# Kernel optimization log

Measured on AMD Instinct MI355X. Metric: run time of the kernel, lower is better.

Reference implementation:

```python
import jax, jax.numpy as jnp
import numpy as np

MAX_DEG = 10
MIN_DEG = 0
N_FEAT = 128
NB_FILTER = 128
BATCH = 128
DEG_COUNT = 30000                      # atoms per degree bucket (static)
N_ATOMS = (MAX_DEG + 1) * DEG_COUNT    # 330000, atoms sorted by degree (deg0 first)
NB_AFFINE = 3 * MAX_DEG + (2 - MIN_DEG)  # 32
EPS = 1e-5


def setup_inputs() -> dict:
    key = jax.random.key(0)
    ks = jax.random.split(key, 16)
    atoms = jax.random.normal(ks[0], (N_ATOMS, N_FEAT), dtype=jnp.float32)
    membership = jax.random.randint(ks[1], (N_ATOMS,), 0, BATCH)
    # deg_slice[d] = [start, count] for degree d (atoms sorted by degree)
    deg_slice = jnp.stack([jnp.arange(MAX_DEG + 1) * DEG_COUNT,
                           jnp.full((MAX_DEG + 1,), DEG_COUNT)], axis=1)
    inp = {"atoms": atoms, "deg_slice": deg_slice, "membership": membership}
    for d in range(1, MAX_DEG + 1):
        inp[f"adj{d}"] = jax.random.randint(ks[1 + d], (DEG_COUNT, d), 0, N_ATOMS)
    glorot = (2.0 / (N_FEAT + NB_FILTER)) ** 0.5
    inp["W"] = jax.random.normal(ks[12], (NB_AFFINE, N_FEAT, NB_FILTER), dtype=jnp.float32) * glorot
    inp["b"] = jnp.zeros((NB_AFFINE, NB_FILTER), dtype=jnp.float32)
    inp["gamma"] = jnp.ones((NB_FILTER,), dtype=jnp.float32)
    inp["beta"] = jnp.zeros((NB_FILTER,), dtype=jnp.float32)
    return inp


def _self_slice(atoms, deg):
    return jax.lax.dynamic_slice_in_dim(atoms, deg * DEG_COUNT, DEG_COUNT, axis=0)


def _norm(x, gamma, beta):
    m = jnp.mean(x, axis=-1, keepdims=True)
    std = jnp.sqrt(jnp.var(x, axis=-1, keepdims=True) + EPS)
    return gamma * ((x - m) / (std + EPS)) + beta


def _forward(atoms, W, b, gamma, beta, membership, adjs):
    # W consumption order matches the TF iterator: for deg=1..max_deg -> (rel, self),
    # then deg0 self at index 2*MAX_DEG, then gather affines deg1..max_deg, deg0 last.
    rel_outs = [None] * (MAX_DEG + 1)
    gather_outs = [None] * (MAX_DEG + 1)
    for d in range(1, MAX_DEG + 1):
        neigh = jnp.sum(atoms[adjs[d - 1]], axis=1)          # (COUNT, F) gather+sum
        self_a = _self_slice(atoms, d)                        # (COUNT, F)
        i_rel, i_self = 2 * (d - 1), 2 * d - 1
        rel_outs[d] = (neigh @ W[i_rel] + b[i_rel]) + (self_a @ W[i_self] + b[i_self])
        i_g = 2 * MAX_DEG + d
        gather_outs[d] = self_a @ W[i_g] + b[i_g]
    self0 = _self_slice(atoms, 0)
    rel_outs[0] = self0 @ W[2 * MAX_DEG] + b[2 * MAX_DEG]
    gather_outs[0] = self0 @ W[NB_AFFINE - 1] + b[NB_AFFINE - 1]

    activated = jnp.concatenate(rel_outs, axis=0)             # (N_ATOMS, NB_FILTER)
    gathered = jnp.concatenate(gather_outs, axis=0)           # (N_ATOMS, NB_FILTER)
    # graph_gather: per-molecule sum (dynamic_partition + reduce_sum)
    atom_gather = jax.ops.segment_sum(gathered, membership, num_segments=BATCH)

    xn = _norm(activated, gamma, beta)                        # per-row "BN" as in source
    yn = _norm(atom_gather, gamma, beta)
    # gather_node: per-molecule max of normalized atom features
    g = jax.ops.segment_max(xn, membership, num_segments=BATCH)
    return xn, yn, g


def reference(atoms, deg_slice, membership, adj1, adj2, adj3, adj4, adj5,
              adj6, adj7, adj8, adj9, adj10, W, b, gamma, beta):
    adjs = (adj1, adj2, adj3, adj4, adj5, adj6, adj7, adj8, adj9, adj10)
    return _forward(atoms, W, b, gamma, beta, membership, adjs)
```

## Files before the change

kernel.cpp:

```cpp
#include <hip/hip_runtime.h>
#include <stdint.h>

#define MAX_DEG   10
#define DEG_COUNT 30000
#define N_ATOMS   330000
#define NF        128
#define BATCH     128
#define SORT_BLOCKS 256
#define SORT_CHUNK  1290
#define NB_BUILD  1408
#define NB_CAST   41250
#define NSLICES   4

typedef __attribute__((ext_vector_type(8))) short bf16x8;
typedef __attribute__((ext_vector_type(4))) float f32x4;
typedef __attribute__((ext_vector_type(2))) float f32x2;

__device__ __forceinline__ float bf2f(unsigned short h) {
  union { unsigned u; float f; } v; v.u = ((unsigned)h) << 16; return v.f;
}
__device__ __forceinline__ unsigned short f2bf(float f) {
  union { float f; unsigned u; } v; v.f = f;
  unsigned u = v.u;
  unsigned r = (u + 0x7fffu + ((u >> 16) & 1u)) >> 16;
  return (unsigned short)r;
}

struct AdjPtrs { const int* p[10]; };

#define NEG_INF_BITS 0xFF800000

__global__ __launch_bounds__(256) void k_prep(
    const float* __restrict__ W,
    const float* __restrict__ b,
    const f32x4* __restrict__ atoms4,
    const int* __restrict__ membership,
    unsigned short* __restrict__ BcatT,
    float* __restrict__ biascat,
    ushort4* __restrict__ dst4,
    int* __restrict__ blockHistT)
{
  const int bx = blockIdx.x;
  const int tid = threadIdx.x;
  __shared__ int bins[BATCH];

  if (bx < NB_BUILD) {
    int idx = bx * 256 + tid;
    if (idx < 11 * 128) {
      int d = idx >> 7, n = idx & 127;
      float f = (d >= 1) ? (b[(2 * (d - 1)) * 128 + n] + b[(2 * d - 1) * 128 + n])
                         : b[20 * 128 + n];
      biascat[idx] = f;
    }
    if (idx < 11 * 128 * 256) {
      int d = idx >> 15;
      int rem = idx & 32767;
      int n = rem >> 8;
      int k = rem & 255;
      float v;
      if (k < 128) {
        v = (d >= 1) ? W[(2 * (d - 1)) * 16384 + k * 128 + n] : 0.f;
      } else {
        int ks = k - 128;
        int wi = (d >= 1) ? (2 * d - 1) : 20;
        v = W[wi * 16384 + ks * 128 + n];
      }
      BcatT[idx] = f2bf(v);
    }
  } else if (bx < NB_BUILD + NB_CAST) {
    size_t i = (size_t)(bx - NB_BUILD) * 256 + tid;
    f32x4 v = __builtin_nontemporal_load(atoms4 + i);
    ushort4 o;
    o.x = f2bf(v[0]); o.y = f2bf(v[1]); o.z = f2bf(v[2]); o.w = f2bf(v[3]);
    dst4[i] = o;
  } else {
    int bh = bx - NB_BUILD - NB_CAST;
    if (tid < BATCH) bins[tid] = 0;
    __syncthreads();
    int lo = bh * SORT_CHUNK, hi = min(lo + SORT_CHUNK, N_ATOMS);
    for (int i = lo + tid; i < hi; i += 256)
      atomicAdd(&bins[membership[i]], 1);
    __syncthreads();
    if (tid < BATCH) blockHistT[tid * 256 + bh] = bins[tid];
  }
}

__global__ __launch_bounds__(256) void k_scan(
    const int* __restrict__ blockHistT,
    int* __restrict__ relOffT,
    int* __restrict__ tot)
{
  const int m = blockIdx.x;
  const int tid = threadIdx.x;
  __shared__ int ws[4];
  int v = blockHistT[m * 256 + tid];
  int x = v;
#pragma unroll
  for (int o = 1; o < 64; o <<= 1) {
    int t = __shfl_up(x, o, 64);
    if ((tid & 63) >= o) x += t;
  }
  if ((tid & 63) == 63) ws[tid >> 6] = x;
  __syncthreads();
  int wb = 0;
  for (int w = 0; w < (tid >> 6); ++w) wb += ws[w];
  int incl = wb + x;
  relOffT[m * 256 + tid] = incl - v;
  if (tid == 255) tot[m] = incl;
}

__global__ __launch_bounds__(256) void k_scatter(
    const int* __restrict__ membership,
    const int* __restrict__ relOffT,
    const int* __restrict__ tot,
    int* __restrict__ perm)
{
  __shared__ int totS[BATCH], baseS[BATCH], bins[BATCH];
  const int tid = threadIdx.x;
  if (tid < BATCH) totS[tid] = tot[tid];
  __syncthreads();
  if (tid == 0) {
    int a = 0;
    for (int i = 0; i < BATCH; ++i) { baseS[i] = a; a += totS[i]; }
  }
  __syncthreads();
  if (tid < BATCH) bins[tid] = baseS[tid] + relOffT[tid * 256 + blockIdx.x];
  __syncthreads();
  int lo = blockIdx.x * SORT_CHUNK, hi = min(lo + SORT_CHUNK, N_ATOMS);
  for (int i = lo + tid; i < hi; i += 256) {
    int m = membership[i];
    int pos = atomicAdd(&bins[m], 1);
    perm[pos] = i;
  }
}

template<int D>
__device__ __forceinline__ void nsum_row1(const unsigned* __restrict__ atomsU,
                                          const int* __restrict__ abase,
                                          unsigned* __restrict__ NS,
                                          int iloc, int rclamp, int lane) {
  const int* a = abase + (size_t)rclamp * D;
  int myIdx = (lane < D) ? a[lane] : 0;
  unsigned xs[D];
#pragma unroll
  for (int j = 0; j < D; ++j) {
    int nbr = __shfl(myIdx, j, 64);
    xs[j] = atomsU[(size_t)nbr * 64 + lane];
  }
  float s0 = 0.f, s1 = 0.f;
#pragma unroll
  for (int j = 0; j < D; ++j) {
    s0 += bf2f((unsigned short)(xs[j] & 0xffff));
    s1 += bf2f((unsigned short)(xs[j] >> 16));
  }
  int sw = lane ^ ((iloc & 7) << 2);
  NS[(size_t)iloc * 64 + sw] = (unsigned)f2bf(s0) | ((unsigned)f2bf(s1) << 16);
}

template<int D>
__device__ __forceinline__ void nsum_phase0(const unsigned* __restrict__ atomsU,
                                            const int* __restrict__ abase,
                                            unsigned* __restrict__ NS,
                                            int rowTile, int wave, int lane) {
  for (int it = 0; it < 4; ++it) {
    int iloc = wave * 16 + it * 4;
    int r0 = rowTile * 128 + iloc;
    if (r0 + 3 < DEG_COUNT) {
      const int* a = abase + (size_t)r0 * D;
      int myIdx = (lane < 4 * D) ? a[lane] : 0;
      unsigned xs[4 * D];
#pragma unroll
      for (int j = 0; j < 4 * D; ++j) {
        int nbr = __shfl(myIdx, j, 64);
        xs[j] = atomsU[(size_t)nbr * 64 + lane];
      }
#pragma unroll
      for (int rr = 0; rr < 4; ++rr) {
        float s0 = 0.f, s1 = 0.f;
#pragma unroll
        for (int j = rr * D; j < (rr + 1) * D; ++j) {
          s0 += bf2f((unsigned short)(xs[j] & 0xffff));
          s1 += bf2f((unsigned short)(xs[j] >> 16));
        }
        int il = iloc + rr;
        int sw = lane ^ ((il & 7) << 2);
        NS[(size_t)il * 64 + sw] = (unsigned)f2bf(s0) | ((unsigned)f2bf(s1) << 16);
      }
    } else {
#pragma unroll
      for (int rr = 0; rr < 4; ++rr) {
        int r = r0 + rr;
        int rc = (r > DEG_COUNT - 1) ? (DEG_COUNT - 1) : r;
        nsum_row1<D>(atomsU, abase, NS, iloc + rr, rc, lane);
      }
    }
  }
}

__global__ __launch_bounds__(512, 4) void k_gemm(
    const unsigned short* __restrict__ atomsBf,
    AdjPtrs adj,
    const unsigned short* __restrict__ BcatT,
    const float* __restrict__ biascat,
    const float* __restrict__ gamma,
    const float* __restrict__ beta,
    float* __restrict__ out0)
{
  const int d = blockIdx.y;
  const int rowTile = blockIdx.x;
  const int tid = threadIdx.x;
  const int lane = tid & 63;
  const int wave = tid >> 6;
  const int m16 = lane & 15;
  const int g = lane >> 4;

  __shared__ unsigned short Bs[128 * 256];
  unsigned* NS = (unsigned*)Bs;

  const unsigned short* Bd = BcatT + d * 32768;
  const unsigned* atomsU = (const unsigned*)atomsBf;

  const int rowBase = rowTile * 128 + wave * 16;
  bf16x8 af[8];
  {
    int rbL = rowBase + m16; if (rbL > DEG_COUNT - 1) rbL = DEG_COUNT - 1;
    size_t gr = (size_t)d * DEG_COUNT + rbL;
#pragma unroll
    for (int ks = 4; ks < 8; ++ks)
      af[ks] = *(const bf16x8*)(atomsBf + gr * 128 + (ks - 4) * 32 + g * 8);
  }

  if (d > 0) {
    const int* abase = adj.p[d - 1];
    switch (d) {
      case 1:  nsum_phase0<1>(atomsU, abase, NS, rowTile, wave, lane); break;
      case 2:  nsum_phase0<2>(atomsU, abase, NS, rowTile, wave, lane); break;
      case 3:  nsum_phase0<3>(atomsU, abase, NS, rowTile, wave, lane); break;
      case 4:  nsum_phase0<4>(atomsU, abase, NS, rowTile, wave, lane); break;
      case 5:  nsum_phase0<5>(atomsU, abase, NS, rowTile, wave, lane); break;
      case 6:  nsum_phase0<6>(atomsU, abase, NS, rowTile, wave, lane); break;
      case 7:  nsum_phase0<7>(atomsU, abase, NS, rowTile, wave, lane); break;
      case 8:  nsum_phase0<8>(atomsU, abase, NS, rowTile, wave, lane); break;
      case 9:  nsum_phase0<9>(atomsU, abase, NS, rowTile, wave, lane); break;
      default: nsum_phase0<10>(atomsU, abase, NS, rowTile, wave, lane); break;
    }
    __syncthreads();
    const char* nsb = (const char*)NS;
    const int rowb = (wave * 16 + m16) * 256;
    const int sw = (m16 & 7) << 4;
#pragma unroll
    for (int ks = 0; ks < 4; ++ks)
      af[ks] = *(const bf16x8*)(nsb + ((rowb + ks * 64 + g * 16) ^ sw));
    __syncthreads();
  } else {
    bf16x8 z = {0, 0, 0, 0, 0, 0, 0, 0};
#pragma unroll
    for (int ks = 0; ks < 4; ++ks) af[ks] = z;
  }

#pragma unroll
  for (int it = 0; it < 8; ++it) {
    int flat = it * 512 + tid;
    int row = flat >> 5;
    int c = flat & 31;
    uint4 v = *(const uint4*)(Bd + row * 256 + c * 8);
    int kb = (c * 16) ^ ((row & 7) << 4);
    *(uint4*)((char*)Bs + row * 512 + kb) = v;
  }

  __syncthreads();

  const int ldsMask = (m16 & 7) << 4;

  f32x4 acc[8];
#pragma unroll
  for (int ct = 0; ct < 8; ++ct) acc[ct] = (f32x4){0.f, 0.f, 0.f, 0.f};

#pragma unroll
  for (int ct = 0; ct < 8; ++ct) {
    const char* bbase = (const char*)Bs + (ct * 16 + m16) * 512;
    bf16x8 bf[8];
#pragma unroll
    for (int ks = 0; ks < 8; ++ks)
      bf[ks] = *(const bf16x8*)(bbase + ((ks * 64 + g * 16) ^ ldsMask));
#pragma unroll
    for (int ks = 0; ks < 8; ++ks)
      acc[ct] = __builtin_amdgcn_mfma_f32_16x16x32_bf16(af[ks], bf[ks], acc[ct], 0, 0, 0);
  }

  float bias_[8], gam[8], bet[8];
#pragma unroll
  for (int ct = 0; ct < 8; ++ct) {
    bias_[ct] = biascat[d * 128 + ct * 16 + m16];
    gam[ct] = gamma[ct * 16 + m16];
    bet[ct] = beta[ct * 16 + m16];
  }

#pragma unroll
  for (int ct = 0; ct < 8; ++ct)
#pragma unroll
    for (int r = 0; r < 4; ++r) acc[ct][r] += bias_[ct];

  float s[4], qq[4];
#pragma unroll
  for (int r = 0; r < 4; ++r) {
    s[r] = 0.f; qq[r] = 0.f;
#pragma unroll
    for (int ct = 0; ct < 8; ++ct) {
      float v = acc[ct][r];
      s[r] += v; qq[r] += v * v;
    }
  }
#pragma unroll
  for (int off = 8; off >= 1; off >>= 1) {
#pragma unroll
    for (int r = 0; r < 4; ++r) {
      s[r]  += __shfl_xor(s[r],  off, 64);
      qq[r] += __shfl_xor(qq[r], off, 64);
    }
  }

#pragma unroll
  for (int r = 0; r < 4; ++r) {
    int rb = rowBase + g * 4 + r;
    float mean = s[r] * (1.0f / 128.0f);
    float var  = qq[r] * (1.0f / 128.0f) - mean * mean;
    float inv  = 1.0f / (sqrtf(var + 1e-5f) + 1e-5f);
    if (rb < DEG_COUNT) {
      size_t grow = (size_t)d * DEG_COUNT + rb;
#pragma unroll
      for (int ct = 0; ct < 8; ++ct)
        out0[grow * 128 + ct * 16 + m16] = gam[ct] * ((acc[ct][r] - mean) * inv) + bet[ct];
    }
  }
}

__global__ __launch_bounds__(512) void k_mreduce(
    const f32x2* __restrict__ xnV,
    const unsigned* __restrict__ atomsU,
    const int* __restrict__ perm,
    const int* __restrict__ tot,
    float* __restrict__ Spart,
    int* __restrict__ cntPart,
    float2* __restrict__ pmax4)
{
  const int m = blockIdx.x >> 2;
  const int s = blockIdx.x & 3;
  const int wave = threadIdx.x >> 6, lane = threadIdx.x & 63;

  __shared__ float S[8][11][128];
  __shared__ int C[8][11];
  __shared__ float2 maxT[8][64];
  __shared__ int totS[BATCH];
  __shared__ int rangeS[2];
  for (int e = lane; e < 11 * 128; e += 64) S[wave][e >> 7][e & 127] = 0.f;
  if (lane < 11) C[wave][lane] = 0;
  if (threadIdx.x < BATCH) totS[threadIdx.x] = tot[threadIdx.x];
  __syncthreads();
  if (threadIdx.x == 0) {
    int a = 0;
    for (int i = 0; i < m; ++i) a += totS[i];
    rangeS[0] = a; rangeS[1] = totS[m];
  }
  __syncthreads();
  const int b0 = rangeS[0], cnt = rangeS[1];
  const int lo = b0 + (cnt * s) / NSLICES;
  const int hi = b0 + (cnt * (s + 1)) / NSLICES;

  const float NEG_INF = __int_as_float((int)NEG_INF_BITS);
  float mx0 = NEG_INF, mx1 = NEG_INF;

  for (int i = lo + wave * 2; i < hi; i += 16) {
    int r0 = perm[i];
    bool has1 = (i + 1 < hi);
    int r1 = has1 ? perm[i + 1] : r0;
    f32x2 x0 = __builtin_nontemporal_load(xnV + (size_t)r0 * 64 + lane);
    unsigned a0 = __builtin_nontemporal_load(atomsU + (size_t)r0 * 64 + lane);
    f32x2 x1 = __builtin_nontemporal_load(xnV + (size_t)r1 * 64 + lane);
    unsigned a1 = __builtin_nontemporal_load(atomsU + (size_t)r1 * 64 + lane);
    int d0 = r0 / DEG_COUNT;
    mx0 = fmaxf(mx0, x0[0]);
    mx1 = fmaxf(mx1, x0[1]);
    S[wave][d0][lane]      += bf2f((unsigned short)(a0 & 0xffff));
    S[wave][d0][64 + lane] += bf2f((unsigned short)(a0 >> 16));
    if (lane == 0) C[wave][d0]++;
    if (has1) {
      int d1 = r1 / DEG_COUNT;
      mx0 = fmaxf(mx0, x1[0]);
      mx1 = fmaxf(mx1, x1[1]);
      S[wave][d1][lane]      += bf2f((unsigned short)(a1 & 0xffff));
      S[wave][d1][64 + lane] += bf2f((unsigned short)(a1 >> 16));
      if (lane == 0) C[wave][d1]++;
    }
  }
  maxT[wave][lane] = make_float2(mx0, mx1);
  __syncthreads();

  if (threadIdx.x < 64) {
    int l = threadIdx.x;
    float2 mm = maxT[0][l];
#pragma unroll
    for (int w = 1; w < 8; ++w) {
      float2 b = maxT[w][l]; mm.x = fmaxf(mm.x, b.x); mm.y = fmaxf(mm.y, b.y);
    }
    pmax4[((size_t)s * 128 + m) * 64 + l] = mm;
  }
  for (int e = threadIdx.x; e < 11 * 128; e += 512) {
    int d = e >> 7, p = e & 127;
    float t = 0.f;
#pragma unroll
    for (int w = 0; w < 8; ++w) t += S[w][d][p];
    int col = (p < 64) ? (2 * p) : (2 * (p - 64) + 1);
    Spart[(((size_t)s * 128 + m) * 11 + d) * 128 + col] = t;
  }
  if (threadIdx.x < 11) {
    int t = 0;
#pragma unroll
    for (int w = 0; w < 8; ++w) t += C[w][threadIdx.x];
    cntPart[((size_t)s * 128 + m) * 11 + threadIdx.x] = t;
  }
}

__global__ __launch_bounds__(128) void k_ynfinal(
    const float* __restrict__ Spart,
    const int* __restrict__ cntPart,
    const float* __restrict__ W,
    const float* __restrict__ b,
    const float* __restrict__ gamma,
    const float* __restrict__ beta,
    const float* __restrict__ pmax4,
    float* __restrict__ out1,
    float* __restrict__ out2)
{
  int m = blockIdx.x;
  int j = threadIdx.x;

  float g = __int_as_float((int)NEG_INF_BITS);
#pragma unroll
  for (int sl = 0; sl < NSLICES; ++sl)
    g = fmaxf(g, pmax4[((size_t)sl * 128 + m) * 128 + j]);
  out2[m * 128 + j] = g;

  __shared__ float Sm[11][128];
  __shared__ float cw[11];
  for (int e = j; e < 11 * 128; e += 128) {
    int d = e >> 7, c = e & 127;
    float t = 0.f;
#pragma unroll
    for (int sl = 0; sl < NSLICES; ++sl)
      t += Spart[(((size_t)sl * 128 + m) * 11 + d) * 128 + c];
    Sm[d][c] = t;
  }
  if (j < 11) {
    int t = 0;
#pragma unroll
    for (int sl = 0; sl < NSLICES; ++sl)
      t += cntPart[((size_t)sl * 128 + m) * 11 + j];
    cw[j] = (float)t;
  }
  __syncthreads();

  float acc = 0.f;
  for (int d = 0; d < 11; ++d) {
    int wi = (d >= 1) ? (20 + d) : 31;
    const float* Wd = W + wi * 16384;
    float a0 = 0.f, a1 = 0.f, a2 = 0.f, a3 = 0.f;
    for (int k = 0; k < 128; k += 4) {
      a0 += Sm[d][k]     * Wd[k * 128 + j];
      a1 += Sm[d][k + 1] * Wd[(k + 1) * 128 + j];
      a2 += Sm[d][k + 2] * Wd[(k + 2) * 128 + j];
      a3 += Sm[d][k + 3] * Wd[(k + 3) * 128 + j];
    }
    acc += (a0 + a1) + (a2 + a3);
    acc += cw[d] * b[wi * 128 + j];
  }

  float ws_ = acc, wq = acc * acc;
#pragma unroll
  for (int off = 32; off >= 1; off >>= 1) {
    ws_ += __shfl_xor(ws_, off, 64);
    wq  += __shfl_xor(wq, off, 64);
  }
  __shared__ float red[4];
  int wave = j >> 6, lane = j & 63;
  if (lane == 0) { red[wave * 2] = ws_; red[wave * 2 + 1] = wq; }
  __syncthreads();
  float Ssum = red[0] + red[2], Q = red[1] + red[3];
  float mean = Ssum * (1.f / 128.f);
  float var = Q * (1.f / 128.f) - mean * mean;
  float inv = 1.f / (sqrtf(var + 1e-5f) + 1e-5f);
  out1[m * 128 + j] = gamma[j] * ((acc - mean) * inv) + beta[j];
}

extern "C" void kernel_launch(void* const* d_in, const int* in_sizes, int n_in,
                              void* d_out, int out_size, void* d_ws, size_t ws_size,
                              hipStream_t stream) {
  const float* atoms = (const float*)d_in[0];
  const int* membership = (const int*)d_in[2];
  AdjPtrs adj;
  for (int i = 0; i < 10; ++i) adj.p[i] = (const int*)d_in[3 + i];
  const float* W     = (const float*)d_in[13];
  const float* b     = (const float*)d_in[14];
  const float* gamma = (const float*)d_in[15];
  const float* beta  = (const float*)d_in[16];

  char* ws = (char*)d_ws;
  size_t off = 0;
  unsigned short* atomsBf = (unsigned short*)(ws + off); off += (size_t)N_ATOMS * 128 * 2;
  unsigned short* BcatT   = (unsigned short*)(ws + off); off += (size_t)11 * 128 * 256 * 2;
  float* biascat          = (float*)(ws + off);          off += (size_t)11 * 128 * 4;
  int* perm               = (int*)(ws + off);            off += (size_t)N_ATOMS * 4;
  int* tot                = (int*)(ws + off);            off += 512;
  int* blockHistT         = (int*)(ws + off);            off += (size_t)BATCH * SORT_BLOCKS * 4;
  int* relOffT            = (int*)(ws + off);            off += (size_t)BATCH * SORT_BLOCKS * 4;
  float* Spart            = (float*)(ws + off);          off += (size_t)NSLICES * 128 * 11 * 128 * 4;
  int* cntPart            = (int*)(ws + off);            off += (size_t)NSLICES * 128 * 11 * 4;
  float* pmax4            = (float*)(ws + off);          off += (size_t)NSLICES * 128 * 128 * 4;

  float* out0 = (float*)d_out;
  float* out1 = out0 + (size_t)N_ATOMS * 128;
  float* out2 = out1 + 16384;

  hipLaunchKernelGGL(k_prep, dim3(NB_BUILD + NB_CAST + SORT_BLOCKS), dim3(256), 0, stream,
                     W, b, (const f32x4*)atoms, membership,
                     BcatT, biascat, (ushort4*)atomsBf, blockHistT);
  hipLaunchKernelGGL(k_scan, dim3(128), dim3(256), 0, stream, blockHistT, relOffT, tot);
  hipLaunchKernelGGL(k_scatter, dim3(SORT_BLOCKS), dim3(256), 0, stream,
                     membership, relOffT, tot, perm);
  hipLaunchKernelGGL(k_gemm, dim3(236, 11), dim3(512), 0, stream,
                     atomsBf, adj, BcatT, biascat, gamma, beta, out0);
  hipLaunchKernelGGL(k_mreduce, dim3(128 * NSLICES), dim3(512), 0, stream,
                     (const f32x2*)out0, (const unsigned*)atomsBf, perm, tot,
                     Spart, cntPart, (float2*)pmax4);
  hipLaunchKernelGGL(k_ynfinal, dim3(128), dim3(128), 0, stream,
                     Spart, cntPart, W, b, gamma, beta, pmax4, out1, out2);
}
```

Before: 492.5 us.

## Widen cast per thread, interleave degree blocks in gemm grid, unroll mreduce loads

The bf16 cast blocks now each handle two float4 elements per thread, halving the number of cast blocks. The gemm grid is flattened so consecutive blocks cycle through degrees, mixing the heavy high-degree gather tiles with light ones across CUs. The per-molecule reduce loop now loads four rows per wave per iteration instead of two, exposing more memory-level parallelism for the random row gathers. Register use rises slightly and load balance depends on scheduling order.

```diff
diff --git a/kernel.cpp b/kernel.cpp
--- a/kernel.cpp
+++ b/kernel.cpp
@@ -9,7 +9,7 @@
 #define SORT_BLOCKS 256
 #define SORT_CHUNK  1290
 #define NB_BUILD  1408
-#define NB_CAST   41250
+#define NB_CAST   20625
 #define NSLICES   4
 
 typedef __attribute__((ext_vector_type(8))) short bf16x8;
@@ -68,11 +68,14 @@
       BcatT[idx] = f2bf(v);
     }
   } else if (bx < NB_BUILD + NB_CAST) {
-    size_t i = (size_t)(bx - NB_BUILD) * 256 + tid;
-    f32x4 v = __builtin_nontemporal_load(atoms4 + i);
-    ushort4 o;
-    o.x = f2bf(v[0]); o.y = f2bf(v[1]); o.z = f2bf(v[2]); o.w = f2bf(v[3]);
-    dst4[i] = o;
+    size_t base = (size_t)(bx - NB_BUILD) * 512 + tid;
+    f32x4 v0 = __builtin_nontemporal_load(atoms4 + base);
+    f32x4 v1 = __builtin_nontemporal_load(atoms4 + base + 256);
+    ushort4 o0, o1;
+    o0.x = f2bf(v0[0]); o0.y = f2bf(v0[1]); o0.z = f2bf(v0[2]); o0.w = f2bf(v0[3]);
+    o1.x = f2bf(v1[0]); o1.y = f2bf(v1[1]); o1.z = f2bf(v1[2]); o1.w = f2bf(v1[3]);
+    dst4[base] = o0;
+    dst4[base + 256] = o1;
   } else {
     int bh = bx - NB_BUILD - NB_CAST;
     if (tid < BATCH) bins[tid] = 0;
@@ -206,8 +209,9 @@
     const float* __restrict__ beta,
     float* __restrict__ out0)
 {
-  const int d = blockIdx.y;
-  const int rowTile = blockIdx.x;
+  const int bid = blockIdx.x;
+  const int d = bid % 11;
+  const int rowTile = bid / 11;
   const int tid = threadIdx.x;
   const int lane = tid & 63;
   const int wave = tid >> 6;
@@ -370,27 +374,30 @@
   const float NEG_INF = __int_as_float((int)NEG_INF_BITS);
   float mx0 = NEG_INF, mx1 = NEG_INF;
 
-  for (int i = lo + wave * 2; i < hi; i += 16) {
-    int r0 = perm[i];
-    bool has1 = (i + 1 < hi);
-    int r1 = has1 ? perm[i + 1] : r0;
-    f32x2 x0 = __builtin_nontemporal_load(xnV + (size_t)r0 * 64 + lane);
-    unsigned a0 = __builtin_nontemporal_load(atomsU + (size_t)r0 * 64 + lane);
-    f32x2 x1 = __builtin_nontemporal_load(xnV + (size_t)r1 * 64 + lane);
-    unsigned a1 = __builtin_nontemporal_load(atomsU + (size_t)r1 * 64 + lane);
-    int d0 = r0 / DEG_COUNT;
-    mx0 = fmaxf(mx0, x0[0]);
-    mx1 = fmaxf(mx1, x0[1]);
-    S[wave][d0][lane]      += bf2f((unsigned short)(a0 & 0xffff));
-    S[wave][d0][64 + lane] += bf2f((unsigned short)(a0 >> 16));
-    if (lane == 0) C[wave][d0]++;
-    if (has1) {
-      int d1 = r1 / DEG_COUNT;
-      mx0 = fmaxf(mx0, x1[0]);
-      mx1 = fmaxf(mx1, x1[1]);
-      S[wave][d1][lane]      += bf2f((unsigned short)(a1 & 0xffff));
-      S[wave][d1][64 + lane] += bf2f((unsigned short)(a1 >> 16));
-      if (lane == 0) C[wave][d1]++;
+  for (int i = lo + wave * 4; i < hi; i += 32) {
+    int rr[4];
+    bool hv[4];
+#pragma unroll
+    for (int k = 0; k < 4; ++k) {
+      hv[k] = (i + k < hi);
+      rr[k] = hv[k] ? perm[i + k] : perm[i];
+    }
+    f32x2 xx[4];
+    unsigned aa[4];
+#pragma unroll
+    for (int k = 0; k < 4; ++k) {
+      xx[k] = __builtin_nontemporal_load(xnV + (size_t)rr[k] * 64 + lane);
+      aa[k] = __builtin_nontemporal_load(atomsU + (size_t)rr[k] * 64 + lane);
+    }
+#pragma unroll
+    for (int k = 0; k < 4; ++k) {
+      if (!hv[k]) continue;
+      int dk = rr[k] / DEG_COUNT;
+      mx0 = fmaxf(mx0, xx[k][0]);
+      mx1 = fmaxf(mx1, xx[k][1]);
+      S[wave][dk][lane]      += bf2f((unsigned short)(aa[k] & 0xffff));
+      S[wave][dk][64 + lane] += bf2f((unsigned short)(aa[k] >> 16));
+      if (lane == 0) C[wave][dk]++;
     }
   }
   maxT[wave][lane] = make_float2(mx0, mx1);
@@ -527,7 +534,7 @@
   hipLaunchKernelGGL(k_scan, dim3(128), dim3(256), 0, stream, blockHistT, relOffT, tot);
   hipLaunchKernelGGL(k_scatter, dim3(SORT_BLOCKS), dim3(256), 0, stream,
                      membership, relOffT, tot, perm);
-  hipLaunchKernelGGL(k_gemm, dim3(236, 11), dim3(512), 0, stream,
+  hipLaunchKernelGGL(k_gemm, dim3(236 * 11), dim3(512), 0, stream,
                      atomsBf, adj, BcatT, biascat, gamma, beta, out0);
   hipLaunchKernelGGL(k_mreduce, dim3(128 * NSLICES), dim3(512), 0, stream,
                      (const f32x2*)out0, (const unsigned*)atomsBf, perm, tot,
```

Result: faster. 475.0 us (-3.6%).
